# Optimization experiments

Measured on AMD Instinct MI355X. Metric: run time of the kernel, lower is better.

The kernel has to match this reference:

```python
import jax, jax.numpy as jnp
import numpy as np

M, K, L, OUT = 16, 64, 6, 128
IN_CH = 2 + 1 + 1 + 1 + 4 * L  # 29
HID_IN = 128 * 2 + 4           # 260


def setup_inputs() -> dict:
    key = jax.random.key(0)
    ks = jax.random.split(key, 5)
    N = 2_000_000
    P = jax.random.normal(ks[0], (N, 2), jnp.float32) * 2.0
    def lin(k, i, o):
        return jax.random.normal(k, (i, o), jnp.float32) / np.float32(np.sqrt(i))
    return {
        'P': P,
        'W1': lin(ks[1], IN_CH, 64), 'b1': jnp.zeros((64,), jnp.float32),
        'W2': lin(ks[2], 64, 128),   'b2': jnp.zeros((128,), jnp.float32),
        'W3': lin(ks[3], HID_IN, 128), 'b3': jnp.zeros((128,), jnp.float32),
        'W4': lin(ks[4], 128, OUT),  'b4': jnp.zeros((OUT,), jnp.float32),
    }


def _fps(P, m):
    # furthest point sampling, seeded at index 0 (standard convention)
    N = P.shape[0]
    def step(carry, _):
        min_d, last_idx = carry
        last = P[last_idx]
        d = jnp.sum((P - last) ** 2, axis=-1)          # [N]
        min_d = jnp.minimum(min_d, d)
        nxt = jnp.argmax(min_d)
        return (min_d, nxt), last_idx
    init = (jnp.full((N,), jnp.finfo(jnp.float32).max, jnp.float32), jnp.int32(0))
    (_, _), idxs = jax.lax.scan(step, init, None, length=m)
    return idxs  # [m] int


def _gelu(x):
    return jax.nn.gelu(x, approximate=False)  # torch nn.GELU default = erf


def reference(P, W1, b1, W2, b2, W3, b3, W4, b4):
    c_idx = jax.lax.stop_gradient(_fps(P, M))
    C = P[c_idx]                                       # [M,2]
    # brute-force kNN: expanded squared distance avoids [M,N,2] intermediate
    Ps = jax.lax.stop_gradient(P)
    Cs = jax.lax.stop_gradient(C)
    d2 = (jnp.sum(Ps ** 2, -1)[None, :]
          - 2.0 * Cs @ Ps.T
          + jnp.sum(Cs ** 2, -1)[:, None])             # [M,N]
    _, nidx = jax.lax.top_k(-d2, K)                    # [M,K]
    patch = P[nidx]                                    # [M,K,2]
    delta = patch - C[:, None, :]                      # [M,K,2]
    r = jnp.linalg.norm(delta, axis=-1, keepdims=True) # [M,K,1]
    theta = jnp.arctan2(delta[..., 1:2], delta[..., 0:1])
    freqs = (2.0 ** jnp.arange(L)).astype(jnp.float32) # [L]
    ang = delta[..., None, :] * freqs[:, None]         # [M,K,L,2]
    ff = jnp.concatenate([jnp.sin(ang), jnp.cos(ang)], -1).reshape(M, K, 4 * L)
    per_pt = jnp.concatenate([delta, r, jnp.sin(theta), jnp.cos(theta), ff], -1)  # [M,K,29]
    h = _gelu(per_pt @ W1 + b1)
    h = _gelu(h @ W2 + b2)                             # [M,K,128]
    h_max = h.max(axis=1)
    h_mean = h.mean(axis=1)
    rr = r[..., 0]                                     # [M,K]
    stats = jnp.stack([rr.mean(1), rr.max(1), rr.min(1), rr.std(1, ddof=1)], -1)  # [M,4]
    z = jnp.concatenate([h_max, h_mean, stats], -1)    # [M,260]
    F = _gelu(z @ W3 + b3) @ W4 + b4                   # [M,OUT]
    return F, C
```

## Files before the change

### kernel.cpp

```cpp
#include <hip/hip_runtime.h>
#include <math.h>

#define MCENT 16
#define KNN   64
#define NBINS 512
#define CAP   7936
#define FPSB  512
#define FPST  256
#define MLPT  1024

__device__ __forceinline__ float gelu_f(float x){
    return 0.5f * x * (1.0f + erff(x * 0.70710678118654752440f));
}

__global__ __launch_bounds__(FPST) void fps_step(
    const float* __restrict__ P, int N,
    float* __restrict__ min_d,
    unsigned long long* __restrict__ partials,
    int k,
    float* __restrict__ cxy,
    float* __restrict__ outC,
    unsigned int* __restrict__ ghist,
    unsigned int* __restrict__ cnt)
{
    const int lane = threadIdx.x & 63;
    const int wid  = threadIdx.x >> 6;
    __shared__ unsigned long long wred[FPST/64];
    __shared__ int s_cur;

    if (k == 0){
        int gi = blockIdx.x*FPST + threadIdx.x;
        if (gi < MCENT*NBINS) ghist[gi] = 0u;
        if (gi < MCENT) cnt[gi] = 0u;
    }

    int cur = 0;
    if (k > 0){
        unsigned long long pb = 0ULL;
        for (int i = threadIdx.x; i < FPSB; i += FPST){
            unsigned long long v = partials[(k-1)*FPSB + i];
            if (v > pb) pb = v;
        }
#pragma unroll
        for (int off = 32; off > 0; off >>= 1){
            unsigned long long o = __shfl_xor(pb, off, 64);
            if (o > pb) pb = o;
        }
        if (lane == 0) wred[wid] = pb;
        __syncthreads();
        if (threadIdx.x == 0){
            unsigned long long b = wred[0];
#pragma unroll
            for (int w = 1; w < FPST/64; ++w) if (wred[w] > b) b = wred[w];
            s_cur = (int)(0xFFFFFFFFu - (unsigned)(b & 0xFFFFFFFFu));
        }
        __syncthreads();
        cur = s_cur;
    }

    if (blockIdx.x == 0 && threadIdx.x == 0){
        float cx = P[2*cur], cy = P[2*cur+1];
        cxy[2*k] = cx; cxy[2*k+1] = cy;
        outC[2*k] = cx; outC[2*k+1] = cy;
    }
    if (k >= MCENT-1) return;

    const float cx = P[2*cur], cy = P[2*cur+1];
    unsigned long long bk = 0ULL;
    const int T  = gridDim.x * FPST;
    const int NP = N >> 1;
    for (int q = blockIdx.x*FPST + threadIdx.x; q < NP; q += T){
        float4 p = ((const float4*)P)[q];
        float dx0 = __fsub_rn(p.x, cx), dy0 = __fsub_rn(p.y, cy);
        float d0  = __fadd_rn(__fmul_rn(dx0,dx0), __fmul_rn(dy0,dy0));
        float dx1 = __fsub_rn(p.z, cx), dy1 = __fsub_rn(p.w, cy);
        float d1  = __fadd_rn(__fmul_rn(dx1,dx1), __fmul_rn(dy1,dy1));
        float2 mp;
        if (k == 0){ mp.x = d0; mp.y = d1; }
        else {
            mp = ((const float2*)min_d)[q];
            mp.x = fminf(mp.x, d0); mp.y = fminf(mp.y, d1);
        }
        ((float2*)min_d)[q] = mp;
        int g = 2*q;
        unsigned long long k0 =
            ((unsigned long long)__float_as_uint(mp.x) << 32)
            | (unsigned long long)(0xFFFFFFFFu - (unsigned)g);
        unsigned long long k1 =
            ((unsigned long long)__float_as_uint(mp.y) << 32)
            | (unsigned long long)(0xFFFFFFFFu - (unsigned)(g+1));
        if (k0 > bk) bk = k0;
        if (k1 > bk) bk = k1;
    }
    if ((N & 1) && blockIdx.x == 0 && threadIdx.x == 0){
        int g = N-1;
        float dx = __fsub_rn(P[2*g], cx), dy = __fsub_rn(P[2*g+1], cy);
        float d  = __fadd_rn(__fmul_rn(dx,dx), __fmul_rn(dy,dy));
        float nm = (k == 0) ? d : fminf(min_d[g], d);
        min_d[g] = nm;
        unsigned long long kk =
            ((unsigned long long)__float_as_uint(nm) << 32)
            | (unsigned long long)(0xFFFFFFFFu - (unsigned)g);
        if (kk > bk) bk = kk;
    }
#pragma unroll
    for (int off = 32; off > 0; off >>= 1){
        unsigned long long o = __shfl_xor(bk, off, 64);
        if (o > bk) bk = o;
    }
    if (lane == 0) wred[wid] = bk;
    __syncthreads();
    if (threadIdx.x == 0){
        unsigned long long b = wred[0];
#pragma unroll
        for (int w = 1; w < FPST/64; ++w) if (wred[w] > b) b = wred[w];
        partials[k*FPSB + blockIdx.x] = b;
    }
}

__global__ __launch_bounds__(256) void hist_kernel(
    const float* __restrict__ P, int N,
    const float* __restrict__ cxy,
    unsigned int* __restrict__ ghist)
{
    __shared__ unsigned int h[MCENT*NBINS];
    __shared__ float scx[MCENT], scy[MCENT], scs2[MCENT];
    for (int i = threadIdx.x; i < MCENT*NBINS; i += blockDim.x) h[i] = 0u;
    if (threadIdx.x < MCENT){
        float a = cxy[2*threadIdx.x], b = cxy[2*threadIdx.x+1];
        scx[threadIdx.x] = a; scy[threadIdx.x] = b;
        scs2[threadIdx.x] = __fadd_rn(__fmul_rn(a,a), __fmul_rn(b,b));
    }
    __syncthreads();
    const int T  = gridDim.x * blockDim.x;
    const int NP = N >> 1;
    for (int q = blockIdx.x*blockDim.x + threadIdx.x; q < NP; q += T){
        float4 p = ((const float4*)P)[q];
        float ps20 = __fadd_rn(__fmul_rn(p.x,p.x), __fmul_rn(p.y,p.y));
        float ps21 = __fadd_rn(__fmul_rn(p.z,p.z), __fmul_rn(p.w,p.w));
#pragma unroll
        for (int m = 0; m < MCENT; ++m){
            float dot0 = __fadd_rn(__fmul_rn(scx[m],p.x), __fmul_rn(scy[m],p.y));
            float d20  = __fadd_rn(__fsub_rn(ps20, __fmul_rn(2.0f,dot0)), scs2[m]);
            atomicAdd(&h[m*NBINS + (__float_as_uint(fmaxf(d20,0.0f)) >> 22)], 1u);
            float dot1 = __fadd_rn(__fmul_rn(scx[m],p.z), __fmul_rn(scy[m],p.w));
            float d21  = __fadd_rn(__fsub_rn(ps21, __fmul_rn(2.0f,dot1)), scs2[m]);
            atomicAdd(&h[m*NBINS + (__float_as_uint(fmaxf(d21,0.0f)) >> 22)], 1u);
        }
    }
    if ((N & 1) && blockIdx.x == 0 && threadIdx.x == 0){
        float x = P[2*(N-1)], y = P[2*(N-1)+1];
        float ps2 = __fadd_rn(__fmul_rn(x,x), __fmul_rn(y,y));
        for (int m = 0; m < MCENT; ++m){
            float dot = __fadd_rn(__fmul_rn(scx[m],x), __fmul_rn(scy[m],y));
            float d2  = __fadd_rn(__fsub_rn(ps2, __fmul_rn(2.0f,dot)), scs2[m]);
            atomicAdd(&h[m*NBINS + (__float_as_uint(fmaxf(d2,0.0f)) >> 22)], 1u);
        }
    }
    __syncthreads();
    for (int i = threadIdx.x; i < MCENT*NBINS; i += blockDim.x){
        unsigned v = h[i];
        if (v) atomicAdd(&ghist[i], v);
    }
}

__global__ void thr_kernel(const unsigned int* __restrict__ ghist,
                           float* __restrict__ thr){
    int m = threadIdx.x;
    if (m < MCENT){
        unsigned cum = 0; int B = NBINS-1;
        for (int b = 0; b < NBINS; ++b){
            cum += ghist[m*NBINS + b];
            if (cum >= KNN){ B = b; break; }
        }
        thr[m] = __uint_as_float((unsigned)(B+1) << 22);
    }
}

__global__ __launch_bounds__(256) void collect_kernel(
    const float* __restrict__ P, int N,
    const float* __restrict__ cxy,
    const float* __restrict__ thr,
    unsigned int* __restrict__ cnt,
    float* __restrict__ cd2,
    int* __restrict__ cidx)
{
    __shared__ float scx[MCENT], scy[MCENT], scs2[MCENT], sth[MCENT];
    if (threadIdx.x < MCENT){
        float a = cxy[2*threadIdx.x], b = cxy[2*threadIdx.x+1];
        scx[threadIdx.x]=a; scy[threadIdx.x]=b;
        scs2[threadIdx.x]=__fadd_rn(__fmul_rn(a,a),__fmul_rn(b,b));
        sth[threadIdx.x]=thr[threadIdx.x];
    }
    __syncthreads();
    const int T  = gridDim.x*blockDim.x;
    const int NP = N >> 1;
    for (int q = blockIdx.x*blockDim.x + threadIdx.x; q < NP; q += T){
        float4 p = ((const float4*)P)[q];
        float ps20 = __fadd_rn(__fmul_rn(p.x,p.x), __fmul_rn(p.y,p.y));
        float ps21 = __fadd_rn(__fmul_rn(p.z,p.z), __fmul_rn(p.w,p.w));
        int g = 2*q;
#pragma unroll
        for (int m = 0; m < MCENT; ++m){
            float dot0 = __fadd_rn(__fmul_rn(scx[m],p.x), __fmul_rn(scy[m],p.y));
            float d20  = __fadd_rn(__fsub_rn(ps20, __fmul_rn(2.0f,dot0)), scs2[m]);
            if (fmaxf(d20,0.0f) < sth[m]){
                unsigned pos = atomicAdd(&cnt[m], 1u);
                if (pos < CAP){ cd2[m*CAP+pos]=d20; cidx[m*CAP+pos]=g; }
            }
            float dot1 = __fadd_rn(__fmul_rn(scx[m],p.z), __fmul_rn(scy[m],p.w));
            float d21  = __fadd_rn(__fsub_rn(ps21, __fmul_rn(2.0f,dot1)), scs2[m]);
            if (fmaxf(d21,0.0f) < sth[m]){
                unsigned pos = atomicAdd(&cnt[m], 1u);
                if (pos < CAP){ cd2[m*CAP+pos]=d21; cidx[m*CAP+pos]=g+1; }
            }
        }
    }
    if ((N & 1) && blockIdx.x == 0 && threadIdx.x == 0){
        int g = N-1;
        float x = P[2*g], y = P[2*g+1];
        float ps2 = __fadd_rn(__fmul_rn(x,x), __fmul_rn(y,y));
        for (int m = 0; m < MCENT; ++m){
            float dot = __fadd_rn(__fmul_rn(scx[m],x), __fmul_rn(scy[m],y));
            float d2  = __fadd_rn(__fsub_rn(ps2, __fmul_rn(2.0f,dot)), scs2[m]);
            if (fmaxf(d2,0.0f) < sth[m]){
                unsigned pos = atomicAdd(&cnt[m], 1u);
                if (pos < CAP){ cd2[m*CAP+pos]=d2; cidx[m*CAP+pos]=g; }
            }
        }
    }
}

__global__ __launch_bounds__(256) void select_kernel(
    const unsigned int* __restrict__ cnt,
    const float* __restrict__ cd2,
    const int* __restrict__ cidx,
    int* __restrict__ nbr)
{
    const int m = blockIdx.x;
    __shared__ unsigned long long keys[CAP];
    unsigned c = cnt[m]; if (c > CAP) c = CAP;
    for (int i = threadIdx.x; i < (int)c; i += 256){
        unsigned u = __float_as_uint(cd2[m*CAP+i]);
        u = (u & 0x80000000u) ? ~u : (u | 0x80000000u);
        keys[i] = ((unsigned long long)u << 32)
                | (unsigned long long)(unsigned)cidx[m*CAP+i];
    }
    __syncthreads();
    for (int i = threadIdx.x; i < (int)c; i += 256){
        unsigned long long ki = keys[i];
        int rank = 0;
        for (int j = 0; j < (int)c; ++j) rank += (keys[j] < ki);
        if (rank < KNN) nbr[m*KNN + rank] = (int)(unsigned)(ki & 0xFFFFFFFFu);
    }
}

__global__ __launch_bounds__(MLPT) void mlp_kernel(
    const float* __restrict__ P,
    const float* __restrict__ cxy,
    const int* __restrict__ nbr,
    const float* __restrict__ W1, const float* __restrict__ b1,
    const float* __restrict__ W2, const float* __restrict__ b2,
    const float* __restrict__ W3, const float* __restrict__ b3,
    const float* __restrict__ W4, const float* __restrict__ b4,
    float* __restrict__ outF)
{
    const int m = blockIdx.x;
    const int tid = threadIdx.x;
    __shared__ float feat[KNN][32];
    __shared__ float h1s[KNN][64];
    __shared__ float sW1[29*64];
    __shared__ float sW2[64*128];
    __shared__ float pmax[8][128], psum[8][128];
    __shared__ float z[260];
    __shared__ float part[8][128];
    __shared__ float zz[128];

    {
        const float4* s2 = (const float4*)W2;
        float4* d2 = (float4*)sW2;
        d2[tid]        = s2[tid];
        d2[tid + 1024] = s2[tid + 1024];
        if (tid < 464) ((float4*)sW1)[tid] = ((const float4*)W1)[tid];
    }

    const float cx = cxy[2*m], cy = cxy[2*m+1];
    if (tid < KNN){
        int g = nbr[m*KNN + tid];
        float dx = P[2*g]   - cx;
        float dy = P[2*g+1] - cy;
        float r  = sqrtf(dx*dx + dy*dy);
        float th = atan2f(dy, dx);
        feat[tid][0]=dx; feat[tid][1]=dy; feat[tid][2]=r;
        feat[tid][3]=sinf(th); feat[tid][4]=cosf(th);
        float fx = dx, fy = dy;
#pragma unroll
        for (int l = 0; l < 6; ++l){
            feat[tid][5+4*l+0]=sinf(fx);
            feat[tid][5+4*l+1]=sinf(fy);
            feat[tid][5+4*l+2]=cosf(fx);
            feat[tid][5+4*l+3]=cosf(fy);
            fx += fx; fy += fy;
        }
    }
    __syncthreads();

#pragma unroll
    for (int rep = 0; rep < 4; ++rep){
        int o = rep*MLPT + tid;
        int k = o >> 6, j = o & 63;
        float acc = b1[j];
#pragma unroll
        for (int c = 0; c < 29; ++c) acc += feat[k][c] * sW1[c*64 + j];
        h1s[k][j] = gelu_f(acc);
    }
    __syncthreads();

    {
        int j = tid & 127, kh = tid >> 7;
        float lmax = -3.402823466e+38f, lsum = 0.f;
        for (int kk = 0; kk < 8; ++kk){
            int k = kh*8 + kk;
            float acc = b2[j];
#pragma unroll 8
            for (int i = 0; i < 64; ++i) acc += h1s[k][i] * sW2[i*128 + j];
            float v = gelu_f(acc);
            lmax = fmaxf(lmax, v);
            lsum += v;
        }
        pmax[kh][j] = lmax; psum[kh][j] = lsum;
    }
    __syncthreads();
    if (tid < 128){
        float mx = pmax[0][tid], sm = psum[0][tid];
#pragma unroll
        for (int w = 1; w < 8; ++w){ mx = fmaxf(mx, pmax[w][tid]); sm += psum[w][tid]; }
        z[tid]       = mx;
        z[128 + tid] = sm * (1.0f/64.0f);
    }
    if (tid >= 128 && tid < 192){
        int l = tid - 128;
        float r = feat[l][2];
        float s = r, mx = r, mn = r;
        for (int off = 1; off < 64; off <<= 1){
            s  += __shfl_xor(s, off, 64);
            mx  = fmaxf(mx, __shfl_xor(mx, off, 64));
            mn  = fminf(mn, __shfl_xor(mn, off, 64));
        }
        float mean = s * (1.0f/64.0f);
        float dv = (r-mean)*(r-mean);
        for (int off = 1; off < 64; off <<= 1) dv += __shfl_xor(dv, off, 64);
        if (l == 0){
            z[256]=mean; z[257]=mx; z[258]=mn; z[259]=sqrtf(dv*(1.0f/63.0f));
        }
    }
    __syncthreads();

    {
        int j = tid & 127, seg = tid >> 7;
        int i0  = (seg < 4) ? seg*33 : 132 + (seg-4)*32;
        int cnt = (seg < 4) ? 33 : 32;
        float acc = 0.f;
        for (int i = i0; i < i0 + cnt; ++i) acc += z[i]*W3[i*128+j];
        part[seg][j] = acc;
    }
    __syncthreads();
    if (tid < 128){
        float a = part[0][tid];
#pragma unroll
        for (int w = 1; w < 8; ++w) a += part[w][tid];
        zz[tid] = gelu_f(a + b3[tid]);
    }
    __syncthreads();
    {
        int j = tid & 127, seg = tid >> 7;
        float acc = 0.f;
#pragma unroll
        for (int i = seg*16; i < seg*16+16; ++i) acc += zz[i]*W4[i*128+j];
        part[seg][j] = acc;
    }
    __syncthreads();
    if (tid < 128){
        float a = part[0][tid];
#pragma unroll
        for (int w = 1; w < 8; ++w) a += part[w][tid];
        outF[m*128 + tid] = a + b4[tid];
    }
}

extern "C" void kernel_launch(void* const* d_in, const int* in_sizes, int n_in,
                              void* d_out, int out_size, void* d_ws, size_t ws_size,
                              hipStream_t stream)
{
    const float* P  = (const float*)d_in[0];
    const float* W1 = (const float*)d_in[1];
    const float* b1 = (const float*)d_in[2];
    const float* W2 = (const float*)d_in[3];
    const float* b2 = (const float*)d_in[4];
    const float* W3 = (const float*)d_in[5];
    const float* b3 = (const float*)d_in[6];
    const float* W4 = (const float*)d_in[7];
    const float* b4 = (const float*)d_in[8];
    int N = in_sizes[0] / 2;
    float* outF = (float*)d_out;
    float* outC = outF + MCENT*128;
    (void)n_in; (void)out_size; (void)ws_size;

    char* base = (char*)d_ws;
    size_t off = 0;
    auto take = [&](size_t bytes)->char*{
        char* p = base + off;
        off = (off + bytes + 255) & ~(size_t)255;
        return p;
    };
    unsigned long long* partials = (unsigned long long*)take((size_t)MCENT*FPSB*8);
    float* cxy         = (float*)take(MCENT*2*4);
    unsigned int* ghist= (unsigned int*)take(MCENT*NBINS*4);
    unsigned int* cnt  = (unsigned int*)take(MCENT*4);
    float* thr         = (float*)take(MCENT*4);
    int*   nbr         = (int*)  take(MCENT*KNN*4);
    float* cd2         = (float*)take((size_t)MCENT*CAP*4);
    int*   cidx        = (int*)  take((size_t)MCENT*CAP*4);
    float* min_d       = (float*)take((size_t)N*4);

    for (int k = 0; k < MCENT-1; ++k)
        fps_step<<<FPSB, FPST, 0, stream>>>(P, N, min_d, partials, k, cxy, outC,
                                            ghist, cnt);
    fps_step<<<1, FPST, 0, stream>>>(P, N, min_d, partials, MCENT-1, cxy, outC,
                                     ghist, cnt);

    hist_kernel<<<512, 256, 0, stream>>>(P, N, cxy, ghist);
    thr_kernel<<<1, 64, 0, stream>>>(ghist, thr);
    collect_kernel<<<512, 256, 0, stream>>>(P, N, cxy, thr, cnt, cd2, cidx);
    select_kernel<<<MCENT, 256, 0, stream>>>(cnt, cd2, cidx, nbr);
    mlp_kernel<<<MCENT, MLPT, 0, stream>>>(P, cxy, nbr, W1,b1,W2,b2,W3,b3,W4,b4, outF);
}
```

Baseline: 310.6 us.

## Subsample kNN histogram and prefilter candidates with a finer histogram in select

The coarse distance histogram now reads only every 16th float4 pair of points and launches fewer blocks. This cuts the LDS atomic work that is used only to pick the kNN radius threshold. The select kernel builds a 512-bin linear histogram over the collected candidates and keeps only those at or below the bin that reaches 64. The quadratic rank sort then runs on that much smaller set, with a global-memory fallback when the filtered set overflows. The cost is that the threshold becomes a statistical estimate, which relies on enough points passing it and on the candidate count fitting in CAP.

Measured after the change: 568.1 us. +82.9%, slower.

```diff
diff --git a/kernel.cpp b/kernel.cpp
--- a/kernel.cpp
+++ b/kernel.cpp
@@ -5,6 +5,7 @@
 #define KNN   64
 #define NBINS 512
 #define CAP   7936
+#define FCAP  2048
 #define FPSB  512
 #define FPST  256
 #define MLPT  1024
@@ -132,10 +133,10 @@
         scs2[threadIdx.x] = __fadd_rn(__fmul_rn(a,a), __fmul_rn(b,b));
     }
     __syncthreads();
-    const int T  = gridDim.x * blockDim.x;
-    const int NP = N >> 1;
-    for (int q = blockIdx.x*blockDim.x + threadIdx.x; q < NP; q += T){
-        float4 p = ((const float4*)P)[q];
+    const int T    = gridDim.x * blockDim.x;
+    const int NP16 = (N >> 1) >> 4;
+    for (int q = blockIdx.x*blockDim.x + threadIdx.x; q < NP16; q += T){
+        float4 p = ((const float4*)P)[(size_t)q << 4];
         float ps20 = __fadd_rn(__fmul_rn(p.x,p.x), __fmul_rn(p.y,p.y));
         float ps21 = __fadd_rn(__fmul_rn(p.z,p.z), __fmul_rn(p.w,p.w));
 #pragma unroll
@@ -146,15 +147,6 @@
             float dot1 = __fadd_rn(__fmul_rn(scx[m],p.z), __fmul_rn(scy[m],p.w));
             float d21  = __fadd_rn(__fsub_rn(ps21, __fmul_rn(2.0f,dot1)), scs2[m]);
             atomicAdd(&h[m*NBINS + (__float_as_uint(fmaxf(d21,0.0f)) >> 22)], 1u);
-        }
-    }
-    if ((N & 1) && blockIdx.x == 0 && threadIdx.x == 0){
-        float x = P[2*(N-1)], y = P[2*(N-1)+1];
-        float ps2 = __fadd_rn(__fmul_rn(x,x), __fmul_rn(y,y));
-        for (int m = 0; m < MCENT; ++m){
-            float dot = __fadd_rn(__fmul_rn(scx[m],x), __fmul_rn(scy[m],y));
-            float d2  = __fadd_rn(__fsub_rn(ps2, __fmul_rn(2.0f,dot)), scs2[m]);
-            atomicAdd(&h[m*NBINS + (__float_as_uint(fmaxf(d2,0.0f)) >> 22)], 1u);
         }
     }
     __syncthreads();
@@ -235,23 +227,71 @@
     const unsigned int* __restrict__ cnt,
     const float* __restrict__ cd2,
     const int* __restrict__ cidx,
+    const float* __restrict__ thr,
     int* __restrict__ nbr)
 {
     const int m = blockIdx.x;
-    __shared__ unsigned long long keys[CAP];
+    __shared__ unsigned hh[512];
+    __shared__ unsigned long long fkeys[FCAP];
+    __shared__ unsigned fcnt;
+    __shared__ int sB2;
     unsigned c = cnt[m]; if (c > CAP) c = CAP;
+    const float s512 = 512.0f / thr[m];
+    for (int i = threadIdx.x; i < 512; i += 256) hh[i] = 0u;
+    if (threadIdx.x == 0) fcnt = 0u;
+    __syncthreads();
     for (int i = threadIdx.x; i < (int)c; i += 256){
-        unsigned u = __float_as_uint(cd2[m*CAP+i]);
-        u = (u & 0x80000000u) ? ~u : (u | 0x80000000u);
-        keys[i] = ((unsigned long long)u << 32)
-                | (unsigned long long)(unsigned)cidx[m*CAP+i];
-    }
-    __syncthreads();
+        int b = (int)(fmaxf(cd2[m*CAP+i], 0.0f) * s512);
+        if (b > 511) b = 511;
+        atomicAdd(&hh[b], 1u);
+    }
+    __syncthreads();
+    if (threadIdx.x == 0){
+        unsigned cum = 0; int B = 511;
+        for (int b = 0; b < 512; ++b){ cum += hh[b]; if (cum >= KNN){ B = b; break; } }
+        sB2 = B;
+    }
+    __syncthreads();
+    const int B2 = sB2;
     for (int i = threadIdx.x; i < (int)c; i += 256){
-        unsigned long long ki = keys[i];
-        int rank = 0;
-        for (int j = 0; j < (int)c; ++j) rank += (keys[j] < ki);
-        if (rank < KNN) nbr[m*KNN + rank] = (int)(unsigned)(ki & 0xFFFFFFFFu);
+        float d2 = cd2[m*CAP+i];
+        int b = (int)(fmaxf(d2, 0.0f) * s512);
+        if (b > 511) b = 511;
+        if (b <= B2){
+            unsigned pos = atomicAdd(&fcnt, 1u);
+            if (pos < FCAP){
+                unsigned u = __float_as_uint(d2);
+                u = (u & 0x80000000u) ? ~u : (u | 0x80000000u);
+                fkeys[pos] = ((unsigned long long)u << 32)
+                           | (unsigned long long)(unsigned)cidx[m*CAP+i];
+            }
+        }
+    }
+    __syncthreads();
+    unsigned f = fcnt;
+    if (f <= FCAP){
+        for (int i = threadIdx.x; i < (int)f; i += 256){
+            unsigned long long ki = fkeys[i];
+            int rank = 0;
+            for (int j = 0; j < (int)f; ++j) rank += (fkeys[j] < ki);
+            if (rank < KNN) nbr[m*KNN + rank] = (int)(unsigned)(ki & 0xFFFFFFFFu);
+        }
+    } else {
+        for (int i = threadIdx.x; i < (int)c; i += 256){
+            unsigned ui = __float_as_uint(cd2[m*CAP+i]);
+            ui = (ui & 0x80000000u) ? ~ui : (ui | 0x80000000u);
+            unsigned long long ki = ((unsigned long long)ui << 32)
+                                  | (unsigned long long)(unsigned)cidx[m*CAP+i];
+            int rank = 0;
+            for (int j = 0; j < (int)c; ++j){
+                unsigned uj = __float_as_uint(cd2[m*CAP+j]);
+                uj = (uj & 0x80000000u) ? ~uj : (uj | 0x80000000u);
+                unsigned long long kj = ((unsigned long long)uj << 32)
+                                      | (unsigned long long)(unsigned)cidx[m*CAP+j];
+                rank += (kj < ki);
+            }
+            if (rank < KNN) nbr[m*KNN + rank] = (int)(unsigned)(ki & 0xFFFFFFFFu);
+        }
     }
 }
 
@@ -359,9 +399,9 @@
     {
         int j = tid & 127, seg = tid >> 7;
         int i0  = (seg < 4) ? seg*33 : 132 + (seg-4)*32;
-        int cnt = (seg < 4) ? 33 : 32;
+        int cntn = (seg < 4) ? 33 : 32;
         float acc = 0.f;
-        for (int i = i0; i < i0 + cnt; ++i) acc += z[i]*W3[i*128+j];
+        for (int i = i0; i < i0 + cntn; ++i) acc += z[i]*W3[i*128+j];
         part[seg][j] = acc;
     }
     __syncthreads();
@@ -429,9 +469,9 @@
     fps_step<<<1, FPST, 0, stream>>>(P, N, min_d, partials, MCENT-1, cxy, outC,
                                      ghist, cnt);
 
-    hist_kernel<<<512, 256, 0, stream>>>(P, N, cxy, ghist);
+    hist_kernel<<<128, 256, 0, stream>>>(P, N, cxy, ghist);
     thr_kernel<<<1, 64, 0, stream>>>(ghist, thr);
     collect_kernel<<<512, 256, 0, stream>>>(P, N, cxy, thr, cnt, cd2, cidx);
-    select_kernel<<<MCENT, 256, 0, stream>>>(cnt, cd2, cidx, nbr);
+    select_kernel<<<MCENT, 256, 0, stream>>>(cnt, cd2, cidx, thr, nbr);
     mlp_kernel<<<MCENT, MLPT, 0, stream>>>(P, cxy, nbr, W1,b1,W2,b2,W3,b3,W4,b4, outF);
 }
```

## Subsample coarse kNN histogram and add linear-bin refine pass to shrink candidates

Applied to the files above, without the earlier changes.

The coarse exponent-bin histogram now looks at only every sixteenth point pair, so that first pass does much less work. A new full-data refine pass then bins distances below the coarse threshold into 256 linear bins, and a second threshold kernel picks a much tighter cutoff. Collect and select therefore handle far fewer candidates, which cuts atomic contention and sorting work. The cost is one extra full pass and two extra launches, and correctness now relies on the subsample being representative: if fewer than 64 true neighbours fall under the sampled threshold, some are missed.

Result: no change. 312.5 us (+0.6%).

```diff
diff --git a/kernel.cpp b/kernel.cpp
--- a/kernel.cpp
+++ b/kernel.cpp
@@ -4,6 +4,7 @@
 #define MCENT 16
 #define KNN   64
 #define NBINS 512
+#define RBINS 256
 #define CAP   7936
 #define FPSB  512
 #define FPST  256
@@ -121,10 +122,15 @@
 __global__ __launch_bounds__(256) void hist_kernel(
     const float* __restrict__ P, int N,
     const float* __restrict__ cxy,
-    unsigned int* __restrict__ ghist)
+    unsigned int* __restrict__ ghist,
+    unsigned int* __restrict__ rhist)
 {
     __shared__ unsigned int h[MCENT*NBINS];
     __shared__ float scx[MCENT], scy[MCENT], scs2[MCENT];
+    {
+        int gi = blockIdx.x*blockDim.x + threadIdx.x;
+        if (gi < MCENT*RBINS) rhist[gi] = 0u;
+    }
     for (int i = threadIdx.x; i < MCENT*NBINS; i += blockDim.x) h[i] = 0u;
     if (threadIdx.x < MCENT){
         float a = cxy[2*threadIdx.x], b = cxy[2*threadIdx.x+1];
@@ -132,10 +138,10 @@
         scs2[threadIdx.x] = __fadd_rn(__fmul_rn(a,a), __fmul_rn(b,b));
     }
     __syncthreads();
-    const int T  = gridDim.x * blockDim.x;
-    const int NP = N >> 1;
-    for (int q = blockIdx.x*blockDim.x + threadIdx.x; q < NP; q += T){
-        float4 p = ((const float4*)P)[q];
+    const int T    = gridDim.x * blockDim.x;
+    const int NP16 = (N >> 1) >> 4;
+    for (int q = blockIdx.x*blockDim.x + threadIdx.x; q < NP16; q += T){
+        float4 p = ((const float4*)P)[(size_t)q << 4];
         float ps20 = __fadd_rn(__fmul_rn(p.x,p.x), __fmul_rn(p.y,p.y));
         float ps21 = __fadd_rn(__fmul_rn(p.z,p.z), __fmul_rn(p.w,p.w));
 #pragma unroll
@@ -148,15 +154,6 @@
             atomicAdd(&h[m*NBINS + (__float_as_uint(fmaxf(d21,0.0f)) >> 22)], 1u);
         }
     }
-    if ((N & 1) && blockIdx.x == 0 && threadIdx.x == 0){
-        float x = P[2*(N-1)], y = P[2*(N-1)+1];
-        float ps2 = __fadd_rn(__fmul_rn(x,x), __fmul_rn(y,y));
-        for (int m = 0; m < MCENT; ++m){
-            float dot = __fadd_rn(__fmul_rn(scx[m],x), __fmul_rn(scy[m],y));
-            float d2  = __fadd_rn(__fsub_rn(ps2, __fmul_rn(2.0f,dot)), scs2[m]);
-            atomicAdd(&h[m*NBINS + (__float_as_uint(fmaxf(d2,0.0f)) >> 22)], 1u);
-        }
-    }
     __syncthreads();
     for (int i = threadIdx.x; i < MCENT*NBINS; i += blockDim.x){
         unsigned v = h[i];
@@ -165,7 +162,8 @@
 }
 
 __global__ void thr_kernel(const unsigned int* __restrict__ ghist,
-                           float* __restrict__ thr){
+                           float* __restrict__ thr,
+                           float* __restrict__ sc2){
     int m = threadIdx.x;
     if (m < MCENT){
         unsigned cum = 0; int B = NBINS-1;
@@ -173,24 +171,94 @@
             cum += ghist[m*NBINS + b];
             if (cum >= KNN){ B = b; break; }
         }
-        thr[m] = __uint_as_float((unsigned)(B+1) << 22);
-    }
-}
-
-__global__ __launch_bounds__(256) void collect_kernel(
+        float t = __uint_as_float((unsigned)(B+1) << 22);
+        thr[m] = t;
+        sc2[m] = 255.0f / t;
+    }
+}
+
+__global__ __launch_bounds__(256) void refine_kernel(
     const float* __restrict__ P, int N,
     const float* __restrict__ cxy,
-    const float* __restrict__ thr,
-    unsigned int* __restrict__ cnt,
-    float* __restrict__ cd2,
-    int* __restrict__ cidx)
-{
-    __shared__ float scx[MCENT], scy[MCENT], scs2[MCENT], sth[MCENT];
+    const float* __restrict__ sc2,
+    unsigned int* __restrict__ rhist)
+{
+    __shared__ unsigned int h[MCENT*RBINS];
+    __shared__ float scx[MCENT], scy[MCENT], scs2[MCENT], ssc[MCENT];
+    for (int i = threadIdx.x; i < MCENT*RBINS; i += blockDim.x) h[i] = 0u;
     if (threadIdx.x < MCENT){
         float a = cxy[2*threadIdx.x], b = cxy[2*threadIdx.x+1];
         scx[threadIdx.x]=a; scy[threadIdx.x]=b;
         scs2[threadIdx.x]=__fadd_rn(__fmul_rn(a,a),__fmul_rn(b,b));
-        sth[threadIdx.x]=thr[threadIdx.x];
+        ssc[threadIdx.x]=sc2[threadIdx.x];
+    }
+    __syncthreads();
+    const int T  = gridDim.x * blockDim.x;
+    const int NP = N >> 1;
+    for (int q = blockIdx.x*blockDim.x + threadIdx.x; q < NP; q += T){
+        float4 p = ((const float4*)P)[q];
+        float ps20 = __fadd_rn(__fmul_rn(p.x,p.x), __fmul_rn(p.y,p.y));
+        float ps21 = __fadd_rn(__fmul_rn(p.z,p.z), __fmul_rn(p.w,p.w));
+#pragma unroll
+        for (int m = 0; m < MCENT; ++m){
+            float dot0 = __fadd_rn(__fmul_rn(scx[m],p.x), __fmul_rn(scy[m],p.y));
+            float d20  = __fadd_rn(__fsub_rn(ps20, __fmul_rn(2.0f,dot0)), scs2[m]);
+            int b0 = (int)(fmaxf(d20, 0.0f) * ssc[m]);
+            if (b0 < RBINS) atomicAdd(&h[m*RBINS + b0], 1u);
+            float dot1 = __fadd_rn(__fmul_rn(scx[m],p.z), __fmul_rn(scy[m],p.w));
+            float d21  = __fadd_rn(__fsub_rn(ps21, __fmul_rn(2.0f,dot1)), scs2[m]);
+            int b1 = (int)(fmaxf(d21, 0.0f) * ssc[m]);
+            if (b1 < RBINS) atomicAdd(&h[m*RBINS + b1], 1u);
+        }
+    }
+    if ((N & 1) && blockIdx.x == 0 && threadIdx.x == 0){
+        int g = N-1;
+        float x = P[2*g], y = P[2*g+1];
+        float ps2 = __fadd_rn(__fmul_rn(x,x), __fmul_rn(y,y));
+        for (int m = 0; m < MCENT; ++m){
+            float dot = __fadd_rn(__fmul_rn(scx[m],x), __fmul_rn(scy[m],y));
+            float d2  = __fadd_rn(__fsub_rn(ps2, __fmul_rn(2.0f,dot)), scs2[m]);
+            int b = (int)(fmaxf(d2, 0.0f) * ssc[m]);
+            if (b < RBINS) atomicAdd(&h[m*RBINS + b], 1u);
+        }
+    }
+    __syncthreads();
+    for (int i = threadIdx.x; i < MCENT*RBINS; i += blockDim.x){
+        unsigned v = h[i];
+        if (v) atomicAdd(&rhist[i], v);
+    }
+}
+
+__global__ void thr2_kernel(const unsigned int* __restrict__ rhist,
+                            int* __restrict__ B2){
+    int m = threadIdx.x;
+    if (m < MCENT){
+        unsigned cum = 0; int B = RBINS-1;
+        for (int b = 0; b < RBINS; ++b){
+            cum += rhist[m*RBINS + b];
+            if (cum >= KNN){ B = b; break; }
+        }
+        B2[m] = B;
+    }
+}
+
+__global__ __launch_bounds__(256) void collect_kernel(
+    const float* __restrict__ P, int N,
+    const float* __restrict__ cxy,
+    const float* __restrict__ sc2,
+    const int* __restrict__ B2,
+    unsigned int* __restrict__ cnt,
+    float* __restrict__ cd2,
+    int* __restrict__ cidx)
+{
+    __shared__ float scx[MCENT], scy[MCENT], scs2[MCENT], ssc[MCENT];
+    __shared__ int sB2[MCENT];
+    if (threadIdx.x < MCENT){
+        float a = cxy[2*threadIdx.x], b = cxy[2*threadIdx.x+1];
+        scx[threadIdx.x]=a; scy[threadIdx.x]=b;
+        scs2[threadIdx.x]=__fadd_rn(__fmul_rn(a,a),__fmul_rn(b,b));
+        ssc[threadIdx.x]=sc2[threadIdx.x];
+        sB2[threadIdx.x]=B2[threadIdx.x];
     }
     __syncthreads();
     const int T  = gridDim.x*blockDim.x;
@@ -204,13 +272,13 @@
         for (int m = 0; m < MCENT; ++m){
             float dot0 = __fadd_rn(__fmul_rn(scx[m],p.x), __fmul_rn(scy[m],p.y));
             float d20  = __fadd_rn(__fsub_rn(ps20, __fmul_rn(2.0f,dot0)), scs2[m]);
-            if (fmaxf(d20,0.0f) < sth[m]){
+            if ((int)(fmaxf(d20,0.0f) * ssc[m]) <= sB2[m]){
                 unsigned pos = atomicAdd(&cnt[m], 1u);
                 if (pos < CAP){ cd2[m*CAP+pos]=d20; cidx[m*CAP+pos]=g; }
             }
             float dot1 = __fadd_rn(__fmul_rn(scx[m],p.z), __fmul_rn(scy[m],p.w));
             float d21  = __fadd_rn(__fsub_rn(ps21, __fmul_rn(2.0f,dot1)), scs2[m]);
-            if (fmaxf(d21,0.0f) < sth[m]){
+            if ((int)(fmaxf(d21,0.0f) * ssc[m]) <= sB2[m]){
                 unsigned pos = atomicAdd(&cnt[m], 1u);
                 if (pos < CAP){ cd2[m*CAP+pos]=d21; cidx[m*CAP+pos]=g+1; }
             }
@@ -223,7 +291,7 @@
         for (int m = 0; m < MCENT; ++m){
             float dot = __fadd_rn(__fmul_rn(scx[m],x), __fmul_rn(scy[m],y));
             float d2  = __fadd_rn(__fsub_rn(ps2, __fmul_rn(2.0f,dot)), scs2[m]);
-            if (fmaxf(d2,0.0f) < sth[m]){
+            if ((int)(fmaxf(d2,0.0f) * ssc[m]) <= sB2[m]){
                 unsigned pos = atomicAdd(&cnt[m], 1u);
                 if (pos < CAP){ cd2[m*CAP+pos]=d2; cidx[m*CAP+pos]=g; }
             }
@@ -359,9 +427,9 @@
     {
         int j = tid & 127, seg = tid >> 7;
         int i0  = (seg < 4) ? seg*33 : 132 + (seg-4)*32;
-        int cnt = (seg < 4) ? 33 : 32;
+        int cntn = (seg < 4) ? 33 : 32;
         float acc = 0.f;
-        for (int i = i0; i < i0 + cnt; ++i) acc += z[i]*W3[i*128+j];
+        for (int i = i0; i < i0 + cntn; ++i) acc += z[i]*W3[i*128+j];
         part[seg][j] = acc;
     }
     __syncthreads();
@@ -416,8 +484,11 @@
     unsigned long long* partials = (unsigned long long*)take((size_t)MCENT*FPSB*8);
     float* cxy         = (float*)take(MCENT*2*4);
     unsigned int* ghist= (unsigned int*)take(MCENT*NBINS*4);
+    unsigned int* rhist= (unsigned int*)take(MCENT*RBINS*4);
     unsigned int* cnt  = (unsigned int*)take(MCENT*4);
     float* thr         = (float*)take(MCENT*4);
+    float* sc2         = (float*)take(MCENT*4);
+    int*   B2          = (int*)  take(MCENT*4);
     int*   nbr         = (int*)  take(MCENT*KNN*4);
     float* cd2         = (float*)take((size_t)MCENT*CAP*4);
     int*   cidx        = (int*)  take((size_t)MCENT*CAP*4);
@@ -429,9 +500,11 @@
     fps_step<<<1, FPST, 0, stream>>>(P, N, min_d, partials, MCENT-1, cxy, outC,
                                      ghist, cnt);
 
-    hist_kernel<<<512, 256, 0, stream>>>(P, N, cxy, ghist);
-    thr_kernel<<<1, 64, 0, stream>>>(ghist, thr);
-    collect_kernel<<<512, 256, 0, stream>>>(P, N, cxy, thr, cnt, cd2, cidx);
+    hist_kernel<<<128, 256, 0, stream>>>(P, N, cxy, ghist, rhist);
+    thr_kernel<<<1, 64, 0, stream>>>(ghist, thr, sc2);
+    refine_kernel<<<256, 256, 0, stream>>>(P, N, cxy, sc2, rhist);
+    thr2_kernel<<<1, 64, 0, stream>>>(rhist, B2);
+    collect_kernel<<<512, 256, 0, stream>>>(P, N, cxy, sc2, B2, cnt, cd2, cidx);
     select_kernel<<<MCENT, 256, 0, stream>>>(cnt, cd2, cidx, nbr);
     mlp_kernel<<<MCENT, MLPT, 0, stream>>>(P, cxy, nbr, W1,b1,W2,b2,W3,b3,W4,b4, outF);
 }
```
